# Performance work log

Hardware: AMD Instinct MI355X
Metric: run time of the kernel (lower is better)

## Reference

```python
import jax, jax.numpy as jnp
import numpy as np

B, LI, LC, H = 16, 2048, 2048, 1024


def setup_inputs() -> dict:
    key = jax.random.key(0)
    k1, k2, k3, k4 = jax.random.split(key, 4)
    inp = jax.random.normal(k1, (B, LI, H), dtype=jnp.float32)
    ctx = jax.random.normal(k2, (B, LC, H), dtype=jnp.float32)
    # mask out the last quarter of context positions (True = masked), never a full row
    context_mask = jnp.broadcast_to(jnp.arange(LC) >= (3 * LC) // 4, (B, LC))
    W = jax.random.normal(k3, (H, H), dtype=jnp.float32) * (1.0 / np.sqrt(H))
    b = jax.random.normal(k4, (H,), dtype=jnp.float32) * 0.01
    return {"input": inp, "context": ctx, "context_mask": context_mask, "W": W, "b": b}


def reference(input, context, context_mask, W, b):
    # shared relu-projected linear for query and key/value sides
    q = jax.nn.relu(jnp.einsum('bih,oh->bio', input, W) + b)    # [B, Li, H]
    k = jax.nn.relu(jnp.einsum('bjh,oh->bjo', context, W) + b)  # [B, Lc, H]
    scores = jnp.einsum('bid,bjd->bij', q, k)                    # [B, Li, Lc], no scaling
    scores = jnp.where(context_mask[:, None, :], -jnp.inf, scores)
    probs = jax.nn.softmax(scores, axis=2)
    return jnp.einsum('bij,bjd->bid', probs, k)                  # weighted sum of context hiddens
```

## Files before the change

### kernel.cpp

```cpp
#include <hip/hip_runtime.h>

typedef _Float16 half8 __attribute__((ext_vector_type(8)));
typedef _Float16 half4 __attribute__((ext_vector_type(4)));
typedef float floatx4 __attribute__((ext_vector_type(4)));

#define OFF_X    0L
#define OFF_S    0L
#define OFF_P    67108864L
#define OFF_W    134217728L
#define OFF_QK   136314880L
#define OFF_KT   270532608L
#define OFF_MASK 337641472L
#define WS_NEED  337674240L

__device__ __forceinline__ void glds16(const void* g, void* l) {
  __builtin_amdgcn_global_load_lds(
      (__attribute__((address_space(1))) void*)(void*)(g),
      (__attribute__((address_space(3))) void*)(l), 16, 0, 0);
}

__global__ void mask_canon(const unsigned* __restrict__ raw,
                           unsigned char* __restrict__ outm) {
  __shared__ int flag;
  int t = threadIdx.x;
  if (t == 0) flag = 0;
  __syncthreads();
  int loc = 0;
  for (int i = t; i < 8192; i += 256)
    if (raw[i] > 1u) loc = 1;
  if (loc) flag = 1;
  __syncthreads();
  if (flag) {
    const unsigned char* b8 = (const unsigned char*)raw;
    for (int j = t; j < 32768; j += 256) outm[j] = (b8[j] != 0);
  } else {
    const int* r32 = (const int*)raw;
    for (int j = t; j < 32768; j += 256) outm[j] = (r32[j] != 0);
  }
}

__global__ __launch_bounds__(256) void cvt_f32_f16(const float* __restrict__ x,
                                                   _Float16* __restrict__ y, long n) {
  long i = ((long)blockIdx.x * 256 + threadIdx.x) * 4;
  if (i + 3 < n) {
    float4 v = *(const float4*)(x + i);
    half4 h;
    h[0] = (_Float16)v.x; h[1] = (_Float16)v.y;
    h[2] = (_Float16)v.z; h[3] = (_Float16)v.w;
    *(half4*)(y + i) = h;
  }
}

template <bool EPI>
__global__ __launch_bounds__(512, 2)
void gemm_nt8(const _Float16* __restrict__ A, long sAz,
              const _Float16* __restrict__ B, long sBz,
              void* __restrict__ Cv, long sCz,
              const float* __restrict__ bias, int K, int ldc) {
  __shared__ _Float16 As[2][256 * 64];
  __shared__ _Float16 Bs[2][256 * 64];
  const int t = threadIdx.x;
  const int l = t & 63;
  const int w = t >> 6;
  const int wr = w >> 2, wc = w & 3;
  A += (long)blockIdx.z * sAz + (long)blockIdx.y * 256 * (long)K;
  B += (long)blockIdx.z * sBz + (long)blockIdx.x * 256 * (long)K;
  const int l15 = l & 15, quad = l >> 4;
  const int srow = l >> 3;
  const int gchunk = (l & 7) ^ (srow & 7);
  const int sbase = w * 8;
  const int cc0 = quad ^ (l15 & 7);
  const int aoff0 = (wr * 128 + l15) * 64 + cc0 * 8;
  const int aoff1 = (wr * 128 + l15) * 64 + (cc0 ^ 4) * 8;
  const int boff0 = (wc * 64 + l15) * 64 + cc0 * 8;
  const int boff1 = (wc * 64 + l15) * 64 + (cc0 ^ 4) * 8;

  floatx4 acc[8][4] = {};
  const int NT = K >> 6;

#define STG(src, dst, rnd, kt)                                                   \
  glds16((src) + (long)((rnd) * 64 + sbase + srow) * K + (kt) + gchunk * 8,      \
         (dst) + ((rnd) * 64 + sbase) * 64)

  STG(A, As[0], 0, 0); STG(A, As[0], 1, 0); STG(A, As[0], 2, 0); STG(A, As[0], 3, 0);
  STG(B, Bs[0], 0, 0); STG(B, Bs[0], 1, 0); STG(B, Bs[0], 2, 0); STG(B, Bs[0], 3, 0);
  {
    const int k1 = (NT > 1) ? 64 : 0;
    STG(B, Bs[1], 0, k1); STG(B, Bs[1], 1, k1); STG(B, Bs[1], 2, k1); STG(B, Bs[1], 3, k1);
  }

#define READ_A(afv, m0)                                           \
  afv[0][0] = *(const half8*)(Ap + aoff0 + (m0) * 1024);          \
  afv[0][1] = *(const half8*)(Ap + aoff1 + (m0) * 1024);          \
  afv[1][0] = *(const half8*)(Ap + aoff0 + ((m0) + 1) * 1024);    \
  afv[1][1] = *(const half8*)(Ap + aoff1 + ((m0) + 1) * 1024);

#define PHASE_TAIL(m0, afv)                                                                                \
  __builtin_amdgcn_s_barrier();                                                                            \
  asm volatile("s_waitcnt lgkmcnt(0)" ::: "memory");                                                       \
  __builtin_amdgcn_s_setprio(1);                                                                           \
  _Pragma("unroll")                                                                                        \
  for (int ni = 0; ni < 4; ++ni) {                                                                         \
    acc[m0][ni] = __builtin_amdgcn_mfma_f32_16x16x32_f16(afv[0][0], bf[ni][0], acc[m0][ni], 0, 0, 0);      \
    acc[m0][ni] = __builtin_amdgcn_mfma_f32_16x16x32_f16(afv[0][1], bf[ni][1], acc[m0][ni], 0, 0, 0);      \
    acc[(m0) + 1][ni] =                                                                                    \
        __builtin_amdgcn_mfma_f32_16x16x32_f16(afv[1][0], bf[ni][0], acc[(m0) + 1][ni], 0, 0, 0);          \
    acc[(m0) + 1][ni] =                                                                                    \
        __builtin_amdgcn_mfma_f32_16x16x32_f16(afv[1][1], bf[ni][1], acc[(m0) + 1][ni], 0, 0, 0);          \
  }                                                                                                        \
  __builtin_amdgcn_s_setprio(0);                                                                           \
  __builtin_amdgcn_s_barrier();

  for (int tt = 0; tt < NT; ++tt) {
    const _Float16* Ap = As[tt & 1];
    const _Float16* Bp = Bs[tt & 1];
    _Float16* Anx = As[(tt + 1) & 1];
    _Float16* Bnx = Bs[tt & 1];
    const int kt1 = ((tt + 1 < NT) ? tt + 1 : NT - 1) * 64;
    const int kt2 = ((tt + 2 < NT) ? tt + 2 : NT - 1) * 64;

    asm volatile("s_waitcnt vmcnt(4)" ::: "memory");
    __builtin_amdgcn_s_barrier();
    asm volatile("" ::: "memory");

    half8 bf[4][2], af0[2][2], af1[2][2];
#pragma unroll
    for (int ni = 0; ni < 4; ++ni) {
      bf[ni][0] = *(const half8*)(Bp + boff0 + ni * 1024);
      bf[ni][1] = *(const half8*)(Bp + boff1 + ni * 1024);
    }
    READ_A(af0, 0)
    STG(A, Anx, 0, kt1);
    STG(A, Anx, 1, kt1);
    PHASE_TAIL(0, af0)
    READ_A(af1, 2)
    STG(A, Anx, 2, kt1);
    STG(A, Anx, 3, kt1);
    PHASE_TAIL(2, af1)
    READ_A(af0, 4)
    STG(B, Bnx, 0, kt2);
    STG(B, Bnx, 1, kt2);
    PHASE_TAIL(4, af0)
    READ_A(af1, 6)
    STG(B, Bnx, 2, kt2);
    STG(B, Bnx, 3, kt2);
    PHASE_TAIL(6, af1)
  }
  asm volatile("s_waitcnt vmcnt(0)" ::: "memory");
#undef STG
#undef READ_A
#undef PHASE_TAIL

  const int rowb = quad * 4;
  const long cbase = (long)blockIdx.z * sCz + (long)blockIdx.y * 256 * (long)ldc + blockIdx.x * 256;
  if constexpr (EPI) {
    _Float16* Cp = (_Float16*)Cv + cbase;
    float bv[4];
#pragma unroll
    for (int ni = 0; ni < 4; ++ni) bv[ni] = bias[blockIdx.x * 256 + wc * 64 + ni * 16 + l15];
#pragma unroll
    for (int mi = 0; mi < 8; ++mi)
#pragma unroll
      for (int ni = 0; ni < 4; ++ni) {
        const int col = wc * 64 + ni * 16 + l15;
#pragma unroll
        for (int p = 0; p < 4; ++p) {
          const int row = wr * 128 + mi * 16 + rowb + p;
          Cp[(long)row * ldc + col] = (_Float16)fmaxf(acc[mi][ni][p] + bv[ni], 0.f);
        }
      }
  } else {
    float* Cp = (float*)Cv + cbase;
#pragma unroll
    for (int mi = 0; mi < 8; ++mi)
#pragma unroll
      for (int ni = 0; ni < 4; ++ni) {
        const int col = wc * 64 + ni * 16 + l15;
#pragma unroll
        for (int p = 0; p < 4; ++p) {
          const int row = wr * 128 + mi * 16 + rowb + p;
          Cp[(long)row * ldc + col] = acc[mi][ni][p];
        }
      }
  }
}

__global__ __launch_bounds__(256) void transpose_k(const _Float16* __restrict__ Km,
                                                   _Float16* __restrict__ KT) {
  __shared__ _Float16 tile[64 * 72];
  const int t = threadIdx.x;
  const long b = blockIdx.z;
  const _Float16* src = Km + (b * 2048 + blockIdx.x * 64) * 1024 + blockIdx.y * 64;
  {
    const int jl = t >> 2, hc = (t & 3) * 16;
    half8 v0 = *(const half8*)(src + (long)jl * 1024 + hc);
    half8 v1 = *(const half8*)(src + (long)jl * 1024 + hc + 8);
    *(half8*)&tile[jl * 72 + hc] = v0;
    *(half8*)&tile[jl * 72 + hc + 8] = v1;
  }
  __syncthreads();
  {
    const int hl = t >> 2, jc = (t & 3) * 16;
    half8 o0, o1;
#pragma unroll
    for (int jj = 0; jj < 8; jj++) o0[jj] = tile[(jc + jj) * 72 + hl];
#pragma unroll
    for (int jj = 0; jj < 8; jj++) o1[jj] = tile[(jc + 8 + jj) * 72 + hl];
    long off = (b * 1024 + blockIdx.y * 64 + hl) * 2048 + blockIdx.x * 64 + jc;
    *(half8*)(KT + off) = o0;
    *(half8*)(KT + off + 8) = o1;
  }
}

__global__ __launch_bounds__(256) void softmax_k(const float* __restrict__ S,
                                                 _Float16* __restrict__ P,
                                                 const unsigned char* __restrict__ mask,
                                                 int b0) {
  const int i = blockIdx.x, z = blockIdx.y, t = threadIdx.x;
  const float* s = S + ((long)z * 2048 + i) * 2048;
  const unsigned char* mrow = mask + (long)(b0 + z) * 2048;
  const int base0 = t * 4, base1 = 1024 + t * 4;
  float4 a0 = *(const float4*)(s + base0);
  float4 a1 = *(const float4*)(s + base1);
  float v[8] = {a0.x, a0.y, a0.z, a0.w, a1.x, a1.y, a1.z, a1.w};
  const float NINF = -__builtin_inff();
#pragma unroll
  for (int k = 0; k < 4; k++) {
    if (mrow[base0 + k]) v[k] = NINF;
    if (mrow[base1 + k]) v[4 + k] = NINF;
  }
  float mx = v[0];
#pragma unroll
  for (int k = 1; k < 8; k++) mx = fmaxf(mx, v[k]);
#pragma unroll
  for (int o = 32; o >= 1; o >>= 1) mx = fmaxf(mx, __shfl_xor(mx, o, 64));
  __shared__ float redm[4], reds[4];
  if ((t & 63) == 0) redm[t >> 6] = mx;
  __syncthreads();
  mx = fmaxf(fmaxf(redm[0], redm[1]), fmaxf(redm[2], redm[3]));
  float e[8], sm = 0.f;
#pragma unroll
  for (int k = 0; k < 8; k++) { e[k] = __expf(v[k] - mx); sm += e[k]; }
#pragma unroll
  for (int o = 32; o >= 1; o >>= 1) sm += __shfl_xor(sm, o, 64);
  if ((t & 63) == 0) reds[t >> 6] = sm;
  __syncthreads();
  sm = reds[0] + reds[1] + reds[2] + reds[3];
  const float inv = 1.0f / sm;
  _Float16* p = P + ((long)z * 2048 + i) * 2048;
  half4 h0, h1;
#pragma unroll
  for (int k = 0; k < 4; k++) { h0[k] = (_Float16)(e[k] * inv); h1[k] = (_Float16)(e[4 + k] * inv); }
  *(half4*)(p + base0) = h0;
  *(half4*)(p + base1) = h1;
}

extern "C" void kernel_launch(void* const* d_in, const int* in_sizes, int n_in,
                              void* d_out, int out_size, void* d_ws, size_t ws_size,
                              hipStream_t stream) {
  (void)in_sizes; (void)n_in; (void)out_size;
  if ((long)ws_size < WS_NEED) return;

  const float* inp  = (const float*)d_in[0];
  const float* ctx  = (const float*)d_in[1];
  const unsigned* msk = (const unsigned*)d_in[2];
  const float* W    = (const float*)d_in[3];
  const float* bias = (const float*)d_in[4];
  float* out = (float*)d_out;
  char* ws = (char*)d_ws;

  _Float16* Xf   = (_Float16*)(ws + OFF_X);
  float*    Sb   = (float*)(ws + OFF_S);
  _Float16* Pb   = (_Float16*)(ws + OFF_P);
  _Float16* Wf   = (_Float16*)(ws + OFF_W);
  _Float16* QK   = (_Float16*)(ws + OFF_QK);
  _Float16* KT   = (_Float16*)(ws + OFF_KT);
  unsigned char* Mc = (unsigned char*)(ws + OFF_MASK);

  mask_canon<<<1, 256, 0, stream>>>(msk, Mc);
  cvt_f32_f16<<<32768, 256, 0, stream>>>(inp, Xf, 33554432L);
  cvt_f32_f16<<<32768, 256, 0, stream>>>(ctx, Xf + 33554432L, 33554432L);
  cvt_f32_f16<<<1024, 256, 0, stream>>>(W, Wf, 1048576L);
  gemm_nt8<true><<<dim3(4, 256, 1), 512, 0, stream>>>(Xf, 0L, Wf, 0L, (void*)QK, 0L,
                                                      bias, 1024, 1024);
  transpose_k<<<dim3(32, 16, 16), 256, 0, stream>>>(QK + 32768L * 1024, KT);
  for (int g = 0; g < 2; g++) {
    for (int q = 0; q < 2; q++) {
      const int bp = g * 2 + q;
      const _Float16* Aq = QK + (long)bp * 4 * 2048 * 1024;
      const _Float16* Bk = QK + (32768L + (long)bp * 4 * 2048) * 1024;
      gemm_nt8<false><<<dim3(8, 8, 4), 512, 0, stream>>>(Aq, 2048L * 1024, Bk, 2048L * 1024,
                                                         (void*)Sb, 2048L * 2048, nullptr,
                                                         1024, 2048);
      softmax_k<<<dim3(2048, 4), 256, 0, stream>>>(Sb, Pb + (long)q * 4 * 2048 * 2048, Mc, bp * 4);
    }
    gemm_nt8<false><<<dim3(4, 8, 8), 512, 0, stream>>>(Pb, 2048L * 2048,
                                                       KT + (long)g * 8 * 1024 * 2048,
                                                       1024L * 2048,
                                                       (void*)(out + (long)g * 8 * 2048 * 1024),
                                                       2048L * 1024, nullptr, 2048, 1024);
  }
}
```

Measured before the change: 984.2 us.

## Fuse fp32-to-fp16 input conversion into projection GEMM and stage epilogue through LDS

The projection GEMM now reads the fp32 input and context directly into registers, converts them to fp16 and writes them into swizzled LDS, so the two large standalone conversion kernels and their fp16 staging buffer go away. The K-loop is restructured into four MFMA phases over a single LDS array with new fragment-loading offsets. The fp16 epilogue is staged through padded LDS to produce coalesced 16-byte stores. In exchange, A-tile loads for the projection become register-mediated instead of async global-to-LDS, and LDS use per block grows, which may reduce overlap or occupancy.

```diff
diff --git a/kernel.cpp b/kernel.cpp
--- a/kernel.cpp
+++ b/kernel.cpp
@@ -4,7 +4,6 @@
 typedef _Float16 half4 __attribute__((ext_vector_type(4)));
 typedef float floatx4 __attribute__((ext_vector_type(4)));
 
-#define OFF_X    0L
 #define OFF_S    0L
 #define OFF_P    67108864L
 #define OFF_W    134217728L
@@ -51,110 +50,187 @@
   }
 }
 
-template <bool EPI>
+template <bool EPI, bool F32A>
 __global__ __launch_bounds__(512, 2)
-void gemm_nt8(const _Float16* __restrict__ A, long sAz,
+void gemm_nt8(const _Float16* __restrict__ A, const float* __restrict__ A0,
+              const float* __restrict__ A1, long sAz,
               const _Float16* __restrict__ B, long sBz,
               void* __restrict__ Cv, long sCz,
               const float* __restrict__ bias, int K, int ldc) {
-  __shared__ _Float16 As[2][256 * 64];
-  __shared__ _Float16 Bs[2][256 * 64];
+  __shared__ _Float16 lds[256 * 264];
   const int t = threadIdx.x;
   const int l = t & 63;
   const int w = t >> 6;
   const int wr = w >> 2, wc = w & 3;
-  A += (long)blockIdx.z * sAz + (long)blockIdx.y * 256 * (long)K;
-  B += (long)blockIdx.z * sBz + (long)blockIdx.x * 256 * (long)K;
   const int l15 = l & 15, quad = l >> 4;
   const int srow = l >> 3;
   const int gchunk = (l & 7) ^ (srow & 7);
   const int sbase = w * 8;
-  const int cc0 = quad ^ (l15 & 7);
-  const int aoff0 = (wr * 128 + l15) * 64 + cc0 * 8;
-  const int aoff1 = (wr * 128 + l15) * 64 + (cc0 ^ 4) * 8;
-  const int boff0 = (wc * 64 + l15) * 64 + cc0 * 8;
-  const int boff1 = (wc * 64 + l15) * 64 + (cc0 ^ 4) * 8;
+
+  const _Float16* Ag = nullptr;
+  const float* Af = nullptr;
+  if constexpr (F32A) {
+    const int hgy = (int)gridDim.y >> 1;
+    Af = ((int)blockIdx.y < hgy) ? A0 + (long)blockIdx.y * 256 * (long)K
+                                 : A1 + (long)((int)blockIdx.y - hgy) * 256 * (long)K;
+  } else {
+    Ag = A + (long)blockIdx.z * sAz + (long)blockIdx.y * 256 * (long)K;
+  }
+  const _Float16* Bg = B + (long)blockIdx.z * sBz + (long)blockIdx.x * 256 * (long)K;
+
+  _Float16* As0 = lds;
+  _Float16* Bs0 = lds + 32768;
+
+  auto aoff = [&](int mi) {
+    const int row = wr * 128 + mi * 16 + l15;
+    return row * 64 + ((quad ^ (row & 7)) << 3);
+  };
+  auto boff = [&](int ni) {
+    const int row = wc * 64 + ni * 16 + l15;
+    return row * 64 + ((quad ^ (row & 7)) << 3);
+  };
+
+  const int frow = t >> 4;
+  const int fcol = (t & 15) * 4;
+  const int fwch = (t & 15) >> 1;
+  const int fsub = (t & 1) * 4;
 
   floatx4 acc[8][4] = {};
+  float4 fA[8];
   const int NT = K >> 6;
 
-#define STG(src, dst, rnd, kt)                                                   \
-  glds16((src) + (long)((rnd) * 64 + sbase + srow) * K + (kt) + gchunk * 8,      \
+#define STGA(dst, rnd, kt)                                                        \
+  glds16(Ag + (long)((rnd) * 64 + sbase + srow) * K + (kt) + gchunk * 8,          \
          (dst) + ((rnd) * 64 + sbase) * 64)
-
-  STG(A, As[0], 0, 0); STG(A, As[0], 1, 0); STG(A, As[0], 2, 0); STG(A, As[0], 3, 0);
-  STG(B, Bs[0], 0, 0); STG(B, Bs[0], 1, 0); STG(B, Bs[0], 2, 0); STG(B, Bs[0], 3, 0);
-  {
-    const int k1 = (NT > 1) ? 64 : 0;
-    STG(B, Bs[1], 0, k1); STG(B, Bs[1], 1, k1); STG(B, Bs[1], 2, k1); STG(B, Bs[1], 3, k1);
-  }
-
-#define READ_A(afv, m0)                                           \
-  afv[0][0] = *(const half8*)(Ap + aoff0 + (m0) * 1024);          \
-  afv[0][1] = *(const half8*)(Ap + aoff1 + (m0) * 1024);          \
-  afv[1][0] = *(const half8*)(Ap + aoff0 + ((m0) + 1) * 1024);    \
-  afv[1][1] = *(const half8*)(Ap + aoff1 + ((m0) + 1) * 1024);
-
-#define PHASE_TAIL(m0, afv)                                                                                \
-  __builtin_amdgcn_s_barrier();                                                                            \
-  asm volatile("s_waitcnt lgkmcnt(0)" ::: "memory");                                                       \
-  __builtin_amdgcn_s_setprio(1);                                                                           \
-  _Pragma("unroll")                                                                                        \
-  for (int ni = 0; ni < 4; ++ni) {                                                                         \
-    acc[m0][ni] = __builtin_amdgcn_mfma_f32_16x16x32_f16(afv[0][0], bf[ni][0], acc[m0][ni], 0, 0, 0);      \
-    acc[m0][ni] = __builtin_amdgcn_mfma_f32_16x16x32_f16(afv[0][1], bf[ni][1], acc[m0][ni], 0, 0, 0);      \
-    acc[(m0) + 1][ni] =                                                                                    \
-        __builtin_amdgcn_mfma_f32_16x16x32_f16(afv[1][0], bf[ni][0], acc[(m0) + 1][ni], 0, 0, 0);          \
-    acc[(m0) + 1][ni] =                                                                                    \
-        __builtin_amdgcn_mfma_f32_16x16x32_f16(afv[1][1], bf[ni][1], acc[(m0) + 1][ni], 0, 0, 0);          \
-  }                                                                                                        \
-  __builtin_amdgcn_s_setprio(0);                                                                           \
-  __builtin_amdgcn_s_barrier();
-
-  for (int tt = 0; tt < NT; ++tt) {
-    const _Float16* Ap = As[tt & 1];
-    const _Float16* Bp = Bs[tt & 1];
-    _Float16* Anx = As[(tt + 1) & 1];
-    _Float16* Bnx = Bs[tt & 1];
-    const int kt1 = ((tt + 1 < NT) ? tt + 1 : NT - 1) * 64;
-    const int kt2 = ((tt + 2 < NT) ? tt + 2 : NT - 1) * 64;
-
+#define STGB(dst, rnd, kt)                                                        \
+  glds16(Bg + (long)((rnd) * 64 + sbase + srow) * K + (kt) + gchunk * 8,          \
+         (dst) + ((rnd) * 64 + sbase) * 64)
+#define PH_SYNC()                                                                 \
+  do {                                                                            \
+    asm volatile("s_waitcnt lgkmcnt(0)" ::: "memory");                            \
+    __builtin_amdgcn_s_barrier();                                                 \
+    __builtin_amdgcn_sched_barrier(8);                   \
+  } while (0)
+#define MM(mh)                                                                    \
+  do {                                                                            \
+    __builtin_amdgcn_s_setprio(1);                                                \
+    _Pragma("unroll") for (int i_ = 0; i_ < 4; ++i_)                              \
+        _Pragma("unroll") for (int n_ = 0; n_ < 4; ++n_)                          \
+            acc[(mh) * 4 + i_][n_] = __builtin_amdgcn_mfma_f32_16x16x32_f16(      \
+                af[i_], bf[n_], acc[(mh) * 4 + i_][n_], 0, 0, 0);                 \
+    __builtin_amdgcn_s_setprio(0);                                                \
+  } while (0)
+
+  if constexpr (F32A) {
+#pragma unroll
+    for (int p = 0; p < 8; ++p)
+      fA[p] = *(const float4*)(Af + (long)(frow + 32 * p) * K + fcol);
+#pragma unroll
+    for (int r = 0; r < 4; ++r) STGB(Bs0, r, 0);
+    {
+      const int k1 = (NT > 1 ? 64 : 0);
+#pragma unroll
+      for (int r = 0; r < 4; ++r) STGB(Bs0 + 16384, r, k1);
+    }
+#pragma unroll
+    for (int p = 0; p < 8; ++p) {
+      half4 h;
+      h[0] = (_Float16)fA[p].x; h[1] = (_Float16)fA[p].y;
+      h[2] = (_Float16)fA[p].z; h[3] = (_Float16)fA[p].w;
+      const int row = frow + 32 * p;
+      *(half4*)(As0 + row * 64 + ((fwch ^ (row & 7)) << 3) + fsub) = h;
+    }
+    asm volatile("s_waitcnt vmcnt(4) lgkmcnt(0)" ::: "memory");
+    __builtin_amdgcn_s_barrier();
+  } else {
+#pragma unroll
+    for (int r = 0; r < 4; ++r) STGA(As0, r, 0);
+#pragma unroll
+    for (int r = 0; r < 4; ++r) STGB(Bs0, r, 0);
+    {
+      const int k1 = (NT > 1 ? 64 : 0);
+#pragma unroll
+      for (int r = 0; r < 4; ++r) STGB(Bs0 + 16384, r, k1);
+    }
     asm volatile("s_waitcnt vmcnt(4)" ::: "memory");
     __builtin_amdgcn_s_barrier();
-    asm volatile("" ::: "memory");
-
-    half8 bf[4][2], af0[2][2], af1[2][2];
-#pragma unroll
-    for (int ni = 0; ni < 4; ++ni) {
-      bf[ni][0] = *(const half8*)(Bp + boff0 + ni * 1024);
-      bf[ni][1] = *(const half8*)(Bp + boff1 + ni * 1024);
-    }
-    READ_A(af0, 0)
-    STG(A, Anx, 0, kt1);
-    STG(A, Anx, 1, kt1);
-    PHASE_TAIL(0, af0)
-    READ_A(af1, 2)
-    STG(A, Anx, 2, kt1);
-    STG(A, Anx, 3, kt1);
-    PHASE_TAIL(2, af1)
-    READ_A(af0, 4)
-    STG(B, Bnx, 0, kt2);
-    STG(B, Bnx, 1, kt2);
-    PHASE_TAIL(4, af0)
-    READ_A(af1, 6)
-    STG(B, Bnx, 2, kt2);
-    STG(B, Bnx, 3, kt2);
-    PHASE_TAIL(6, af1)
+  }
+
+  for (int tt = 0; tt < NT; ++tt) {
+    const _Float16* Ap = As0 + (tt & 1) * 16384;
+    const _Float16* Bp = Bs0 + (tt & 1) * 16384;
+    _Float16* Anx = As0 + ((tt + 1) & 1) * 16384;
+    _Float16* Bnx = Bs0 + (tt & 1) * 16384;
+    const int kt1 = ((tt + 1 < NT) ? tt + 1 : NT - 1) << 6;
+    const int kt2 = ((tt + 2 < NT) ? tt + 2 : NT - 1) << 6;
+    half8 af[4], bf[4];
+
+#pragma unroll
+    for (int ni = 0; ni < 4; ++ni) bf[ni] = *(const half8*)(Bp + boff(ni));
+#pragma unroll
+    for (int i = 0; i < 4; ++i) af[i] = *(const half8*)(Ap + aoff(i));
+    if constexpr (F32A) {
+#pragma unroll
+      for (int p = 0; p < 8; ++p)
+        fA[p] = *(const float4*)(Af + (long)(frow + 32 * p) * K + kt1 + fcol);
+    } else {
+      STGA(Anx, 0, kt1);
+      STGA(Anx, 1, kt1);
+    }
+    PH_SYNC();
+    MM(0);
+
+#pragma unroll
+    for (int i = 0; i < 4; ++i) af[i] = *(const half8*)(Ap + aoff(4 + i));
+    if constexpr (!F32A) {
+      STGA(Anx, 2, kt1);
+      STGA(Anx, 3, kt1);
+    }
+    PH_SYNC();
+    MM(1);
+
+#pragma unroll
+    for (int ni = 0; ni < 4; ++ni) bf[ni] = *(const half8*)(Bp + (boff(ni) ^ 32));
+#pragma unroll
+    for (int i = 0; i < 4; ++i) af[i] = *(const half8*)(Ap + (aoff(i) ^ 32));
+    PH_SYNC();
+    MM(0);
+
+#pragma unroll
+    for (int i = 0; i < 4; ++i) af[i] = *(const half8*)(Ap + (aoff(4 + i) ^ 32));
+    if constexpr (F32A) {
+#pragma unroll
+      for (int p = 0; p < 8; ++p) {
+        half4 h;
+        h[0] = (_Float16)fA[p].x; h[1] = (_Float16)fA[p].y;
+        h[2] = (_Float16)fA[p].z; h[3] = (_Float16)fA[p].w;
+        const int row = frow + 32 * p;
+        *(half4*)(Anx + row * 64 + ((fwch ^ (row & 7)) << 3) + fsub) = h;
+      }
+#pragma unroll
+      for (int r = 0; r < 4; ++r) STGB(Bnx, r, kt2);
+      PH_SYNC();
+      MM(1);
+    } else {
+#pragma unroll
+      for (int r = 0; r < 4; ++r) STGB(Bnx, r, kt2);
+      PH_SYNC();
+      MM(1);
+      asm volatile("s_waitcnt vmcnt(4)" ::: "memory");
+      __builtin_amdgcn_s_barrier();
+    }
   }
   asm volatile("s_waitcnt vmcnt(0)" ::: "memory");
-#undef STG
-#undef READ_A
-#undef PHASE_TAIL
-
+  __syncthreads();
+#undef STGA
+#undef STGB
+#undef PH_SYNC
+#undef MM
+
+  const long cbase = (long)blockIdx.z * sCz + (long)blockIdx.y * 256 * (long)ldc +
+                     (long)blockIdx.x * 256;
   const int rowb = quad * 4;
-  const long cbase = (long)blockIdx.z * sCz + (long)blockIdx.y * 256 * (long)ldc + blockIdx.x * 256;
   if constexpr (EPI) {
-    _Float16* Cp = (_Float16*)Cv + cbase;
     float bv[4];
 #pragma unroll
     for (int ni = 0; ni < 4; ++ni) bv[ni] = bias[blockIdx.x * 256 + wc * 64 + ni * 16 + l15];
@@ -166,9 +242,19 @@
 #pragma unroll
         for (int p = 0; p < 4; ++p) {
           const int row = wr * 128 + mi * 16 + rowb + p;
-          Cp[(long)row * ldc + col] = (_Float16)fmaxf(acc[mi][ni][p] + bv[ni], 0.f);
+          lds[row * 264 + (((col >> 3) ^ (row & 7)) << 3) + (col & 7)] =
+              (_Float16)fmaxf(acc[mi][ni][p] + bv[ni], 0.f);
         }
       }
+    __syncthreads();
+    _Float16* Cp = (_Float16*)Cv + cbase;
+#pragma unroll
+    for (int pp = 0; pp < 16; ++pp) {
+      const int r = (t >> 5) + 16 * pp;
+      const int c = t & 31;
+      half8 v = *(const half8*)(lds + r * 264 + ((c ^ (r & 7)) << 3));
+      *(half8*)(Cp + (long)r * ldc + c * 8) = v;
+    }
   } else {
     float* Cp = (float*)Cv + cbase;
 #pragma unroll
@@ -269,7 +355,6 @@
   float* out = (float*)d_out;
   char* ws = (char*)d_ws;
 
-  _Float16* Xf   = (_Float16*)(ws + OFF_X);
   float*    Sb   = (float*)(ws + OFF_S);
   _Float16* Pb   = (_Float16*)(ws + OFF_P);
   _Float16* Wf   = (_Float16*)(ws + OFF_W);
@@ -278,26 +363,22 @@
   unsigned char* Mc = (unsigned char*)(ws + OFF_MASK);
 
   mask_canon<<<1, 256, 0, stream>>>(msk, Mc);
-  cvt_f32_f16<<<32768, 256, 0, stream>>>(inp, Xf, 33554432L);
-  cvt_f32_f16<<<32768, 256, 0, stream>>>(ctx, Xf + 33554432L, 33554432L);
   cvt_f32_f16<<<1024, 256, 0, stream>>>(W, Wf, 1048576L);
-  gemm_nt8<true><<<dim3(4, 256, 1), 512, 0, stream>>>(Xf, 0L, Wf, 0L, (void*)QK, 0L,
-                                                      bias, 1024, 1024);
+  gemm_nt8<true, true><<<dim3(4, 256, 1), 512, 0, stream>>>(
+      nullptr, inp, ctx, 0L, Wf, 0L, (void*)QK, 0L, bias, 1024, 1024);
   transpose_k<<<dim3(32, 16, 16), 256, 0, stream>>>(QK + 32768L * 1024, KT);
   for (int g = 0; g < 2; g++) {
     for (int q = 0; q < 2; q++) {
       const int bp = g * 2 + q;
       const _Float16* Aq = QK + (long)bp * 4 * 2048 * 1024;
       const _Float16* Bk = QK + (32768L + (long)bp * 4 * 2048) * 1024;
-      gemm_nt8<false><<<dim3(8, 8, 4), 512, 0, stream>>>(Aq, 2048L * 1024, Bk, 2048L * 1024,
-                                                         (void*)Sb, 2048L * 2048, nullptr,
-                                                         1024, 2048);
+      gemm_nt8<false, false><<<dim3(8, 8, 4), 512, 0, stream>>>(
+          Aq, nullptr, nullptr, 2048L * 1024, Bk, 2048L * 1024,
+          (void*)Sb, 2048L * 2048, nullptr, 1024, 2048);
       softmax_k<<<dim3(2048, 4), 256, 0, stream>>>(Sb, Pb + (long)q * 4 * 2048 * 2048, Mc, bp * 4);
     }
-    gemm_nt8<false><<<dim3(4, 8, 8), 512, 0, stream>>>(Pb, 2048L * 2048,
-                                                       KT + (long)g * 8 * 1024 * 2048,
-                                                       1024L * 2048,
-                                                       (void*)(out + (long)g * 8 * 2048 * 1024),
-                                                       2048L * 1024, nullptr, 2048, 1024);
-  }
-}
+    gemm_nt8<false, false><<<dim3(4, 8, 8), 512, 0, stream>>>(
+        Pb, nullptr, nullptr, 2048L * 2048, KT + (long)g * 8 * 1024 * 2048, 1024L * 2048,
+        (void*)(out + (long)g * 8 * 2048 * 1024), 2048L * 1024, nullptr, 2048, 1024);
+  }
+}
```

After: 875.6 us. -11.0%, faster.

## Triple-buffer B tiles, restructure MFMA phases, and stage fp16 epilogue through LDS

Applied to the files above, without the earlier changes.

Rewrites the GEMM main loop to use a single LDS arena holding a double-buffered A tile and a triple-buffered B tile. The k-tile is split into two 32-wide halves, each computed as four phases of a 4x4 MFMA block with reloaded fragments, which changes how the LDS reads interleave with the async global-to-LDS prefetches. The fp16 bias+ReLU epilogue now writes to a swizzled LDS staging buffer and then emits coalesced 16-byte global stores instead of scattered 2-byte stores. LDS use grows to 160KB per block, which may affect occupancy at the requested two blocks per CU. More fragment reloads per k-tile add LDS traffic.

```diff
diff --git a/kernel.cpp b/kernel.cpp
--- a/kernel.cpp
+++ b/kernel.cpp
@@ -53,108 +53,130 @@
 
 template <bool EPI>
 __global__ __launch_bounds__(512, 2)
-void gemm_nt8(const _Float16* __restrict__ A, long sAz,
+void gemm_nt3(const _Float16* __restrict__ A, long sAz,
               const _Float16* __restrict__ B, long sBz,
               void* __restrict__ Cv, long sCz,
               const float* __restrict__ bias, int K, int ldc) {
-  __shared__ _Float16 As[2][256 * 64];
-  __shared__ _Float16 Bs[2][256 * 64];
+  __shared__ _Float16 lds[81920];
   const int t = threadIdx.x;
   const int l = t & 63;
   const int w = t >> 6;
   const int wr = w >> 2, wc = w & 3;
-  A += (long)blockIdx.z * sAz + (long)blockIdx.y * 256 * (long)K;
-  B += (long)blockIdx.z * sBz + (long)blockIdx.x * 256 * (long)K;
   const int l15 = l & 15, quad = l >> 4;
   const int srow = l >> 3;
   const int gchunk = (l & 7) ^ (srow & 7);
   const int sbase = w * 8;
-  const int cc0 = quad ^ (l15 & 7);
-  const int aoff0 = (wr * 128 + l15) * 64 + cc0 * 8;
-  const int aoff1 = (wr * 128 + l15) * 64 + (cc0 ^ 4) * 8;
-  const int boff0 = (wc * 64 + l15) * 64 + cc0 * 8;
-  const int boff1 = (wc * 64 + l15) * 64 + (cc0 ^ 4) * 8;
+
+  const _Float16* Ag = A + (long)blockIdx.z * sAz + (long)blockIdx.y * 256 * (long)K;
+  const _Float16* Bg = B + (long)blockIdx.z * sBz + (long)blockIdx.x * 256 * (long)K;
+
+  _Float16* const As = lds;
+  _Float16* const Bs = lds + 32768;
+
+  const int arow = wr * 128 + l15;
+  const int brow = wc * 64 + l15;
+  const int ccA = (quad ^ (arow & 7)) << 3;
+  const int ccB = (quad ^ (brow & 7)) << 3;
 
   floatx4 acc[8][4] = {};
   const int NT = K >> 6;
 
-#define STG(src, dst, rnd, kt)                                                   \
-  glds16((src) + (long)((rnd) * 64 + sbase + srow) * K + (kt) + gchunk * 8,      \
+#define STG(gp, dst, rnd, kt)                                                  \
+  glds16(gp + (long)((rnd) * 64 + sbase + srow) * K + (kt) + gchunk * 8,       \
          (dst) + ((rnd) * 64 + sbase) * 64)
-
-  STG(A, As[0], 0, 0); STG(A, As[0], 1, 0); STG(A, As[0], 2, 0); STG(A, As[0], 3, 0);
-  STG(B, Bs[0], 0, 0); STG(B, Bs[0], 1, 0); STG(B, Bs[0], 2, 0); STG(B, Bs[0], 3, 0);
+#define MM(mh)                                                                 \
+  do {                                                                         \
+    _Pragma("unroll") for (int mi_ = 0; mi_ < 4; ++mi_)                        \
+      _Pragma("unroll") for (int ni_ = 0; ni_ < 4; ++ni_)                      \
+        acc[(mh) * 4 + mi_][ni_] = __builtin_amdgcn_mfma_f32_16x16x32_f16(     \
+            af[mi_], bf[ni_], acc[(mh) * 4 + mi_][ni_], 0, 0, 0);              \
+  } while (0)
+#define PH_HEAD()                                                              \
+  __builtin_amdgcn_s_barrier();                                                \
+  asm volatile("s_waitcnt lgkmcnt(0)" ::: "memory");                           \
+  __builtin_amdgcn_s_setprio(1)
+#define PH_TAIL()                                                              \
+  __builtin_amdgcn_s_setprio(0)
+
+  STG(Ag, As, 0, 0); STG(Ag, As, 1, 0); STG(Ag, As, 2, 0); STG(Ag, As, 3, 0);
+  STG(Bg, Bs, 0, 0); STG(Bg, Bs, 1, 0); STG(Bg, Bs, 2, 0); STG(Bg, Bs, 3, 0);
   {
-    const int k1 = (NT > 1) ? 64 : 0;
-    STG(B, Bs[1], 0, k1); STG(B, Bs[1], 1, k1); STG(B, Bs[1], 2, k1); STG(B, Bs[1], 3, k1);
-  }
-
-#define READ_A(afv, m0)                                           \
-  afv[0][0] = *(const half8*)(Ap + aoff0 + (m0) * 1024);          \
-  afv[0][1] = *(const half8*)(Ap + aoff1 + (m0) * 1024);          \
-  afv[1][0] = *(const half8*)(Ap + aoff0 + ((m0) + 1) * 1024);    \
-  afv[1][1] = *(const half8*)(Ap + aoff1 + ((m0) + 1) * 1024);
-
-#define PHASE_TAIL(m0, afv)                                                                                \
-  __builtin_amdgcn_s_barrier();                                                                            \
-  asm volatile("s_waitcnt lgkmcnt(0)" ::: "memory");                                                       \
-  __builtin_amdgcn_s_setprio(1);                                                                           \
-  _Pragma("unroll")                                                                                        \
-  for (int ni = 0; ni < 4; ++ni) {                                                                         \
-    acc[m0][ni] = __builtin_amdgcn_mfma_f32_16x16x32_f16(afv[0][0], bf[ni][0], acc[m0][ni], 0, 0, 0);      \
-    acc[m0][ni] = __builtin_amdgcn_mfma_f32_16x16x32_f16(afv[0][1], bf[ni][1], acc[m0][ni], 0, 0, 0);      \
-    acc[(m0) + 1][ni] =                                                                                    \
-        __builtin_amdgcn_mfma_f32_16x16x32_f16(afv[1][0], bf[ni][0], acc[(m0) + 1][ni], 0, 0, 0);          \
-    acc[(m0) + 1][ni] =                                                                                    \
-        __builtin_amdgcn_mfma_f32_16x16x32_f16(afv[1][1], bf[ni][1], acc[(m0) + 1][ni], 0, 0, 0);          \
-  }                                                                                                        \
-  __builtin_amdgcn_s_setprio(0);                                                                           \
+    const int k1 = (NT > 1 ? 64 : 0);
+    _Float16* b1 = Bs + 16384;
+    STG(Bg, b1, 0, k1); STG(Bg, b1, 1, k1); STG(Bg, b1, 2, k1); STG(Bg, b1, 3, k1);
+  }
+  asm volatile("s_waitcnt vmcnt(4)" ::: "memory");
   __builtin_amdgcn_s_barrier();
 
+  int bq = 0, bq2 = 2;
   for (int tt = 0; tt < NT; ++tt) {
-    const _Float16* Ap = As[tt & 1];
-    const _Float16* Bp = Bs[tt & 1];
-    _Float16* Anx = As[(tt + 1) & 1];
-    _Float16* Bnx = Bs[tt & 1];
-    const int kt1 = ((tt + 1 < NT) ? tt + 1 : NT - 1) * 64;
-    const int kt2 = ((tt + 2 < NT) ? tt + 2 : NT - 1) * 64;
-
+    const _Float16* Ap = As + (tt & 1) * 16384;
+    const _Float16* Bp = Bs + bq * 16384;
+    _Float16* Anx = As + ((tt + 1) & 1) * 16384;
+    _Float16* Bnx = Bs + bq2 * 16384;
+    const int kt1 = ((tt + 1 < NT) ? tt + 1 : NT - 1) << 6;
+    const int kt2 = ((tt + 2 < NT) ? tt + 2 : NT - 1) << 6;
+    half8 af[4], bf[4];
+
+#pragma unroll
+    for (int ni = 0; ni < 4; ++ni) bf[ni] = *(const half8*)(Bp + (brow + ni * 16) * 64 + ccB);
+#pragma unroll
+    for (int mi = 0; mi < 4; ++mi) af[mi] = *(const half8*)(Ap + (arow + mi * 16) * 64 + ccA);
+    STG(Ag, Anx, 0, kt1);
+    STG(Ag, Anx, 1, kt1);
+    PH_HEAD();
+    MM(0);
+    PH_TAIL();
+    __builtin_amdgcn_s_barrier();
+
+#pragma unroll
+    for (int mi = 0; mi < 4; ++mi)
+      af[mi] = *(const half8*)(Ap + (arow + (mi + 4) * 16) * 64 + ccA);
+    STG(Ag, Anx, 2, kt1);
+    STG(Ag, Anx, 3, kt1);
+    PH_HEAD();
+    MM(1);
+    PH_TAIL();
+    __builtin_amdgcn_s_barrier();
+
+#pragma unroll
+    for (int ni = 0; ni < 4; ++ni)
+      bf[ni] = *(const half8*)(Bp + (brow + ni * 16) * 64 + (ccB ^ 32));
+#pragma unroll
+    for (int mi = 0; mi < 4; ++mi)
+      af[mi] = *(const half8*)(Ap + (arow + mi * 16) * 64 + (ccA ^ 32));
+    STG(Bg, Bnx, 0, kt2);
+    STG(Bg, Bnx, 1, kt2);
+    PH_HEAD();
+    MM(0);
+    PH_TAIL();
+    __builtin_amdgcn_s_barrier();
+
+#pragma unroll
+    for (int mi = 0; mi < 4; ++mi)
+      af[mi] = *(const half8*)(Ap + (arow + (mi + 4) * 16) * 64 + (ccA ^ 32));
+    STG(Bg, Bnx, 2, kt2);
+    STG(Bg, Bnx, 3, kt2);
+    PH_HEAD();
+    MM(1);
+    PH_TAIL();
     asm volatile("s_waitcnt vmcnt(4)" ::: "memory");
     __builtin_amdgcn_s_barrier();
-    asm volatile("" ::: "memory");
-
-    half8 bf[4][2], af0[2][2], af1[2][2];
-#pragma unroll
-    for (int ni = 0; ni < 4; ++ni) {
-      bf[ni][0] = *(const half8*)(Bp + boff0 + ni * 1024);
-      bf[ni][1] = *(const half8*)(Bp + boff1 + ni * 1024);
-    }
-    READ_A(af0, 0)
-    STG(A, Anx, 0, kt1);
-    STG(A, Anx, 1, kt1);
-    PHASE_TAIL(0, af0)
-    READ_A(af1, 2)
-    STG(A, Anx, 2, kt1);
-    STG(A, Anx, 3, kt1);
-    PHASE_TAIL(2, af1)
-    READ_A(af0, 4)
-    STG(B, Bnx, 0, kt2);
-    STG(B, Bnx, 1, kt2);
-    PHASE_TAIL(4, af0)
-    READ_A(af1, 6)
-    STG(B, Bnx, 2, kt2);
-    STG(B, Bnx, 3, kt2);
-    PHASE_TAIL(6, af1)
+
+    bq = (bq == 2) ? 0 : bq + 1;
+    bq2 = (bq2 == 2) ? 0 : bq2 + 1;
   }
   asm volatile("s_waitcnt vmcnt(0)" ::: "memory");
+  __syncthreads();
 #undef STG
-#undef READ_A
-#undef PHASE_TAIL
-
+#undef MM
+#undef PH_HEAD
+#undef PH_TAIL
+
+  const long cbase = (long)blockIdx.z * sCz + (long)blockIdx.y * 256 * (long)ldc +
+                     (long)blockIdx.x * 256;
   const int rowb = quad * 4;
-  const long cbase = (long)blockIdx.z * sCz + (long)blockIdx.y * 256 * (long)ldc + blockIdx.x * 256;
   if constexpr (EPI) {
-    _Float16* Cp = (_Float16*)Cv + cbase;
     float bv[4];
 #pragma unroll
     for (int ni = 0; ni < 4; ++ni) bv[ni] = bias[blockIdx.x * 256 + wc * 64 + ni * 16 + l15];
@@ -166,9 +188,19 @@
 #pragma unroll
         for (int p = 0; p < 4; ++p) {
           const int row = wr * 128 + mi * 16 + rowb + p;
-          Cp[(long)row * ldc + col] = (_Float16)fmaxf(acc[mi][ni][p] + bv[ni], 0.f);
+          lds[row * 264 + (((col >> 3) ^ (row & 7)) << 3) + (col & 7)] =
+              (_Float16)fmaxf(acc[mi][ni][p] + bv[ni], 0.f);
         }
       }
+    __syncthreads();
+    _Float16* Cp = (_Float16*)Cv + cbase;
+#pragma unroll
+    for (int pp = 0; pp < 16; ++pp) {
+      const int r = (t >> 5) + 16 * pp;
+      const int c = t & 31;
+      half8 v = *(const half8*)(lds + r * 264 + ((c ^ (r & 7)) << 3));
+      *(half8*)(Cp + (long)r * ldc + c * 8) = v;
+    }
   } else {
     float* Cp = (float*)Cv + cbase;
 #pragma unroll
@@ -281,7 +313,7 @@
   cvt_f32_f16<<<32768, 256, 0, stream>>>(inp, Xf, 33554432L);
   cvt_f32_f16<<<32768, 256, 0, stream>>>(ctx, Xf + 33554432L, 33554432L);
   cvt_f32_f16<<<1024, 256, 0, stream>>>(W, Wf, 1048576L);
-  gemm_nt8<true><<<dim3(4, 256, 1), 512, 0, stream>>>(Xf, 0L, Wf, 0L, (void*)QK, 0L,
+  gemm_nt3<true><<<dim3(4, 256, 1), 512, 0, stream>>>(Xf, 0L, Wf, 0L, (void*)QK, 0L,
                                                       bias, 1024, 1024);
   transpose_k<<<dim3(32, 16, 16), 256, 0, stream>>>(QK + 32768L * 1024, KT);
   for (int g = 0; g < 2; g++) {
@@ -289,15 +321,12 @@
       const int bp = g * 2 + q;
       const _Float16* Aq = QK + (long)bp * 4 * 2048 * 1024;
       const _Float16* Bk = QK + (32768L + (long)bp * 4 * 2048) * 1024;
-      gemm_nt8<false><<<dim3(8, 8, 4), 512, 0, stream>>>(Aq, 2048L * 1024, Bk, 2048L * 1024,
-                                                         (void*)Sb, 2048L * 2048, nullptr,
-                                                         1024, 2048);
+      gemm_nt3<false><<<dim3(8, 8, 4), 512, 0, stream>>>(
+          Aq, 2048L * 1024, Bk, 2048L * 1024, (void*)Sb, 2048L * 2048, nullptr, 1024, 2048);
       softmax_k<<<dim3(2048, 4), 256, 0, stream>>>(Sb, Pb + (long)q * 4 * 2048 * 2048, Mc, bp * 4);
     }
-    gemm_nt8<false><<<dim3(4, 8, 8), 512, 0, stream>>>(Pb, 2048L * 2048,
-                                                       KT + (long)g * 8 * 1024 * 2048,
-                                                       1024L * 2048,
-                                                       (void*)(out + (long)g * 8 * 2048 * 1024),
-                                                       2048L * 1024, nullptr, 2048, 1024);
-  }
-}
+    gemm_nt3<false><<<dim3(4, 8, 8), 512, 0, stream>>>(
+        Pb, 2048L * 2048, KT + (long)g * 8 * 1024 * 2048, 1024L * 2048,
+        (void*)(out + (long)g * 8 * 2048 * 1024), 2048L * 1024, nullptr, 2048, 1024);
+  }
+}
```

After: 852.4 us. 1.15x faster.
